# Performance work log

Hardware: AMD Instinct MI355X
Metric: run time of the kernel (lower is better)

The kernel has to match this reference:

```python
import jax, jax.numpy as jnp
import numpy as np

B, C, W, H = 4, 256, 64, 64
DK = C // 8  # query/key channels


def setup_inputs() -> dict:
    key = jax.random.key(0)
    ks = jax.random.split(key, 7)
    x = jax.random.normal(ks[0], (B, C, W, H), dtype=jnp.float32)
    # conv1x1 weights stored as [out_ch, in_ch]
    Wq = jax.random.normal(ks[1], (DK, C), dtype=jnp.float32) / np.sqrt(C)
    bq = jnp.zeros((DK,), dtype=jnp.float32)
    Wk = jax.random.normal(ks[2], (DK, C), dtype=jnp.float32) / np.sqrt(C)
    bk = jnp.zeros((DK,), dtype=jnp.float32)
    Wv = jax.random.normal(ks[3], (C, C), dtype=jnp.float32) / np.sqrt(C)
    bv = jnp.zeros((C,), dtype=jnp.float32)
    gamma = jnp.zeros((1,), dtype=jnp.float32)
    return {"x": x, "Wq": Wq, "bq": bq, "Wk": Wk, "bk": bk,
            "Wv": Wv, "bv": bv, "gamma": gamma}


def reference(x, Wq, bq, Wk, bk, Wv, bv, gamma):
    b, c, w, h = x.shape
    n = w * h
    xf = x.reshape(b, c, n)                     # [B, C, N]
    # conv1x1 == channel matmul
    q = jnp.einsum('dc,bcn->bnd', Wq, xf) + bq  # [B, N, DK]
    k = jnp.einsum('dc,bcn->bdn', Wk, xf) + bk[None, :, None]  # [B, DK, N]
    energy = jnp.einsum('bnd,bdm->bnm', q, k)   # [B, N, N]
    attention = jax.nn.softmax(energy, axis=-1)
    v = jnp.einsum('dc,bcn->bdn', Wv, xf) + bv[None, :, None]  # [B, C, N]
    out = jnp.einsum('bdm,bnm->bdn', v, attention)              # [B, C, N]
    out = out.reshape(b, c, w, h)
    out = gamma * out + x
    return out, attention
```

## Files before the change

kernel.cpp:

```cpp
#include <hip/hip_runtime.h>
#include <hip/hip_bf16.h>

typedef __attribute__((ext_vector_type(8))) short bf16x8;
typedef __attribute__((ext_vector_type(4))) float f32x4;
typedef __attribute__((ext_vector_type(4))) unsigned int u32x4;

#define B_SZ 4
#define C_SZ 256
#define N_SZ 4096
#define DK_SZ 32

#define WQB_OFF 0
#define WKB_OFF 8192
#define WVB_OFF 16384
#define QB_OFF  81920
#define KB_OFF  606208
#define VB_OFF  1130496

__device__ __forceinline__ short f2bf(float f) {
    union { float f; unsigned int u; } v; v.f = f;
    unsigned int r = v.u + 0x7fffu + ((v.u >> 16) & 1u);
    return (short)(r >> 16);
}
__device__ __forceinline__ float bf2f(short s) {
    union { float f; unsigned int u; } v;
    v.u = ((unsigned int)(unsigned short)s) << 16;
    return v.f;
}

__device__ __forceinline__ f32x4 mfma16(bf16x8 a, bf16x8 b, f32x4 c) {
    return __builtin_amdgcn_mfma_f32_16x16x32_bf16(a, b, c, 0, 0, 0);
}

__global__ __launch_bounds__(256) void k_convw(const float* __restrict__ Wq,
                                               const float* __restrict__ Wk,
                                               const float* __restrict__ Wv,
                                               short* __restrict__ ws) {
    int i = blockIdx.x * 256 + threadIdx.x;
    if (i < 8192) {
        ws[WQB_OFF + i] = f2bf(Wq[i]);
        ws[WKB_OFF + i] = f2bf(Wk[i]);
    }
    ws[WVB_OFF + i] = f2bf(Wv[i]);
}

__global__ __launch_bounds__(256) void k_prep(const float* __restrict__ x,
                                              const float* __restrict__ bq,
                                              const float* __restrict__ bk,
                                              const float* __restrict__ bv,
                                              short* __restrict__ ws) {
    __shared__ short xsT[64][264];
    __shared__ short vt_s[64][258];

    const int b = blockIdx.y;
    const int n0 = blockIdx.x * 64;
    const int t = threadIdx.x;
    const float* xb = x + (size_t)b * C_SZ * N_SZ;

    {
        int c0 = t >> 4, n4 = (t & 15) * 4;
#pragma unroll
        for (int i = 0; i < 16; i++) {
            int c = c0 + 16 * i;
            float4 v = *(const float4*)(xb + (size_t)c * N_SZ + n0 + n4);
            xsT[n4 + 0][c] = f2bf(v.x);
            xsT[n4 + 1][c] = f2bf(v.y);
            xsT[n4 + 2][c] = f2bf(v.z);
            xsT[n4 + 3][c] = f2bf(v.w);
        }
    }
    __syncthreads();

    const int w = t >> 6, l = t & 63;
    const int lr = l & 15, lk = l >> 4;

    bf16x8 af[8];
#pragma unroll
    for (int kk = 0; kk < 8; kk++)
        af[kk] = *(const bf16x8*)(&xsT[w * 16 + lr][kk * 32 + lk * 8]);

#pragma unroll
    for (int qk = 0; qk < 2; qk++) {
        const short* wb = ws + (qk ? WKB_OFF : WQB_OFF);
        const float* bias = qk ? bk : bq;
        short* outp = ws + (qk ? KB_OFF : QB_OFF) + (size_t)b * N_SZ * DK_SZ;
#pragma unroll
        for (int cf = 0; cf < 2; cf++) {
            f32x4 acc = {0.f, 0.f, 0.f, 0.f};
#pragma unroll
            for (int kk = 0; kk < 8; kk++) {
                bf16x8 bfr = *(const bf16x8*)(wb + (cf * 16 + lr) * 256 + kk * 32 + lk * 8);
                acc = mfma16(af[kk], bfr, acc);
            }
            float bias_v = bias[cf * 16 + lr];
#pragma unroll
            for (int r = 0; r < 4; r++) {
                int row = w * 16 + lk * 4 + r;
                outp[(size_t)(n0 + row) * DK_SZ + cf * 16 + lr] = f2bf(acc[r] + bias_v);
            }
        }
    }

#pragma unroll
    for (int cf = 0; cf < 16; cf++) {
        f32x4 acc = {0.f, 0.f, 0.f, 0.f};
#pragma unroll
        for (int kk = 0; kk < 8; kk++) {
            bf16x8 bfr = *(const bf16x8*)(ws + WVB_OFF + (cf * 16 + lr) * 256 + kk * 32 + lk * 8);
            acc = mfma16(af[kk], bfr, acc);
        }
        float bias_v = bv[cf * 16 + lr];
#pragma unroll
        for (int r = 0; r < 4; r++) {
            vt_s[w * 16 + lk * 4 + r][cf * 16 + lr] = f2bf(acc[r] + bias_v);
        }
    }
    __syncthreads();
    {
        short* vb = ws + VB_OFF + (size_t)b * C_SZ * N_SZ;
        int nn = t & 63;
#pragma unroll
        for (int i = 0; i < 64; i++) {
            int c = (t >> 6) + 4 * i;
            vb[(size_t)c * N_SZ + n0 + nn] = vt_s[nn][c];
        }
    }
}

__global__ __launch_bounds__(512) void k_attn(const short* __restrict__ ws,
                                              const float* __restrict__ x,
                                              const float* __restrict__ gamma_p,
                                              float* __restrict__ out) {
    __shared__ short v_lds[256][72];
    __shared__ short p_lds[64][72];
    __shared__ float rsum_s[2][64];
    __shared__ float o_s[64][258];

    const int b = blockIdx.y;
    const int n0 = blockIdx.x * 64;
    const int t = threadIdx.x, w = t >> 6, l = t & 63;
    const int rg = w & 3, ch = w >> 2;
    const int lr = l & 15, lk = l >> 4;

    const short* qb = ws + QB_OFF + (size_t)b * N_SZ * DK_SZ;
    const short* kb = ws + KB_OFF + (size_t)b * N_SZ * DK_SZ;
    const short* vb = ws + VB_OFF + (size_t)b * C_SZ * N_SZ;

    bf16x8 qf = *(const bf16x8*)(qb + (size_t)(n0 + rg * 16 + lr) * DK_SZ + lk * 8);

    float rs[4] = {0.f, 0.f, 0.f, 0.f};
    {
        int mb = ch * 32;
        bf16x8 k0 = *(const bf16x8*)(kb + (size_t)(mb + lr) * DK_SZ + lk * 8);
        bf16x8 k1 = *(const bf16x8*)(kb + (size_t)(mb + 16 + lr) * DK_SZ + lk * 8);
        for (int mt = 0; mt < 64; mt++) {
            int mtn = (mt + 1) & 63;
            int mbn = mtn * 64 + ch * 32;
            bf16x8 nk0 = *(const bf16x8*)(kb + (size_t)(mbn + lr) * DK_SZ + lk * 8);
            bf16x8 nk1 = *(const bf16x8*)(kb + (size_t)(mbn + 16 + lr) * DK_SZ + lk * 8);
            f32x4 s0 = {0.f, 0.f, 0.f, 0.f}, s1 = {0.f, 0.f, 0.f, 0.f};
            s0 = mfma16(qf, k0, s0);
            s1 = mfma16(qf, k1, s1);
#pragma unroll
            for (int r = 0; r < 4; r++) rs[r] += __expf(s0[r]) + __expf(s1[r]);
            k0 = nk0; k1 = nk1;
        }
    }
#pragma unroll
    for (int r = 0; r < 4; r++) {
        rs[r] += __shfl_xor(rs[r], 1);
        rs[r] += __shfl_xor(rs[r], 2);
        rs[r] += __shfl_xor(rs[r], 4);
        rs[r] += __shfl_xor(rs[r], 8);
    }
    if (lr == 0) {
#pragma unroll
        for (int r = 0; r < 4; r++) rsum_s[ch][rg * 16 + lk * 4 + r] = rs[r];
    }
    __syncthreads();
    float inv[4];
#pragma unroll
    for (int r = 0; r < 4; r++) {
        int row = rg * 16 + lk * 4 + r;
        inv[r] = 1.f / (rsum_s[0][row] + rsum_s[1][row]);
    }

    float* attn = out + (size_t)B_SZ * C_SZ * N_SZ + (size_t)b * N_SZ * N_SZ;
    f32x4 O[8];
#pragma unroll
    for (int cb = 0; cb < 8; cb++) O[cb] = (f32x4){0.f, 0.f, 0.f, 0.f};

    for (int mt = 0; mt < 64; mt++) {
        int mb = mt * 64;
#pragma unroll
        for (int i = 0; i < 4; i++) {
            int chunk = t + 512 * i;
            int c = chunk >> 3, o8 = chunk & 7;
            u32x4 d = *(const u32x4*)(vb + (size_t)c * N_SZ + mb + o8 * 8);
            *(u32x4*)(&v_lds[c][o8 * 8]) = d;
        }
        {
            int mbh = mb + ch * 32;
            bf16x8 k0 = *(const bf16x8*)(kb + (size_t)(mbh + lr) * DK_SZ + lk * 8);
            bf16x8 k1 = *(const bf16x8*)(kb + (size_t)(mbh + 16 + lr) * DK_SZ + lk * 8);
            f32x4 s0 = {0.f, 0.f, 0.f, 0.f}, s1 = {0.f, 0.f, 0.f, 0.f};
            s0 = mfma16(qf, k0, s0);
            s1 = mfma16(qf, k1, s1);
#pragma unroll
            for (int r = 0; r < 4; r++) {
                int row = rg * 16 + lk * 4 + r;
                p_lds[row][ch * 32 + lr]      = f2bf(__expf(s0[r]) * inv[r]);
                p_lds[row][ch * 32 + 16 + lr] = f2bf(__expf(s1[r]) * inv[r]);
            }
        }
        __syncthreads();
        {
            int n = t >> 3, m8 = (t & 7) * 8;
            bf16x8 pv = *(const bf16x8*)(&p_lds[n][m8]);
            float* dst = attn + (size_t)(n0 + n) * N_SZ + mb + m8;
            float4 f0, f1;
            f0.x = bf2f(pv[0]); f0.y = bf2f(pv[1]); f0.z = bf2f(pv[2]); f0.w = bf2f(pv[3]);
            f1.x = bf2f(pv[4]); f1.y = bf2f(pv[5]); f1.z = bf2f(pv[6]); f1.w = bf2f(pv[7]);
            *(float4*)dst = f0;
            *(float4*)(dst + 4) = f1;
        }
        {
            bf16x8 a0 = *(const bf16x8*)(&p_lds[rg * 16 + lr][lk * 8]);
            bf16x8 a1 = *(const bf16x8*)(&p_lds[rg * 16 + lr][32 + lk * 8]);
#pragma unroll
            for (int cb = 0; cb < 8; cb++) {
                int cc = ch * 128 + cb * 16 + lr;
                bf16x8 b0 = *(const bf16x8*)(&v_lds[cc][lk * 8]);
                bf16x8 b1 = *(const bf16x8*)(&v_lds[cc][32 + lk * 8]);
                O[cb] = mfma16(a0, b0, O[cb]);
                O[cb] = mfma16(a1, b1, O[cb]);
            }
        }
        __syncthreads();
    }

    float g = gamma_p[0];
#pragma unroll
    for (int cb = 0; cb < 8; cb++) {
#pragma unroll
        for (int r = 0; r < 4; r++) {
            o_s[rg * 16 + lk * 4 + r][ch * 128 + cb * 16 + lr] = O[cb][r];
        }
    }
    __syncthreads();
    {
        const float* xb = x + (size_t)b * C_SZ * N_SZ;
        float* ob = out + (size_t)b * C_SZ * N_SZ;
        int nn = t & 63;
#pragma unroll
        for (int i = 0; i < 32; i++) {
            int c = (t >> 6) + 8 * i;
            ob[(size_t)c * N_SZ + n0 + nn] = g * o_s[nn][c] + xb[(size_t)c * N_SZ + n0 + nn];
        }
    }
}

extern "C" void kernel_launch(void* const* d_in, const int* in_sizes, int n_in,
                              void* d_out, int out_size, void* d_ws, size_t ws_size,
                              hipStream_t stream) {
    const float* x     = (const float*)d_in[0];
    const float* Wq    = (const float*)d_in[1];
    const float* bq    = (const float*)d_in[2];
    const float* Wk    = (const float*)d_in[3];
    const float* bk    = (const float*)d_in[4];
    const float* Wv    = (const float*)d_in[5];
    const float* bv    = (const float*)d_in[6];
    const float* gamma = (const float*)d_in[7];
    short* ws = (short*)d_ws;
    float* out = (float*)d_out;

    hipLaunchKernelGGL(k_convw, dim3(256), dim3(256), 0, stream, Wq, Wk, Wv, ws);
    hipLaunchKernelGGL(k_prep, dim3(64, 4), dim3(256), 0, stream, x, bq, bk, bv, ws);
    hipLaunchKernelGGL(k_attn, dim3(64, 4), dim3(512), 0, stream, ws, x, gamma, out);
}
```

Measured before the change: 171.5 us.

## Double-buffer V and P tiles with async global-to-LDS loads in attention kernel

Restructures the attention main loop into a software pipeline. The next V tile is loaded straight into a second LDS buffer with global_load_lds using an XOR-swizzled layout, and the next tile's scores and softmax are computed before the PV MFMAs of the current tile, which removes one barrier per iteration. Attention probabilities are now written to global memory directly from fp32 registers instead of round-tripping through bf16 LDS, and packed bf16 conversion uses v_cvt_pk_bf16_f32. The output staging buffer reuses the V LDS space in two halves to save LDS, and the row-sum pass computes the transposed score tile. The risks are higher register and LDS pressure and the correctness of the swizzle and direct-to-LDS loads.

```diff
diff --git a/kernel.cpp b/kernel.cpp
--- a/kernel.cpp
+++ b/kernel.cpp
@@ -4,6 +4,7 @@
 typedef __attribute__((ext_vector_type(8))) short bf16x8;
 typedef __attribute__((ext_vector_type(4))) float f32x4;
 typedef __attribute__((ext_vector_type(4))) unsigned int u32x4;
+typedef __attribute__((ext_vector_type(2))) unsigned int u32x2;
 
 #define B_SZ 4
 #define C_SZ 256
@@ -22,14 +23,20 @@
     unsigned int r = v.u + 0x7fffu + ((v.u >> 16) & 1u);
     return (short)(r >> 16);
 }
-__device__ __forceinline__ float bf2f(short s) {
-    union { float f; unsigned int u; } v;
-    v.u = ((unsigned int)(unsigned short)s) << 16;
-    return v.f;
+
+__device__ __forceinline__ unsigned int cvt_pk_bf16(float lo, float hi) {
+    unsigned int r;
+    asm volatile("v_cvt_pk_bf16_f32 %0, %1, %2" : "=v"(r) : "v"(lo), "v"(hi));
+    return r;
 }
 
 __device__ __forceinline__ f32x4 mfma16(bf16x8 a, bf16x8 b, f32x4 c) {
     return __builtin_amdgcn_mfma_f32_16x16x32_bf16(a, b, c, 0, 0, 0);
+}
+
+__device__ __forceinline__ void gload_lds16(const void* g, void* l) {
+    __builtin_amdgcn_global_load_lds((const __attribute__((address_space(1))) unsigned int*)g,
+                                     (__attribute__((address_space(3))) unsigned int*)l, 16, 0, 0);
 }
 
 __global__ __launch_bounds__(256) void k_convw(const float* __restrict__ Wq,
@@ -127,14 +134,13 @@
     }
 }
 
-__global__ __launch_bounds__(512) void k_attn(const short* __restrict__ ws,
-                                              const float* __restrict__ x,
-                                              const float* __restrict__ gamma_p,
-                                              float* __restrict__ out) {
-    __shared__ short v_lds[256][72];
-    __shared__ short p_lds[64][72];
+__global__ __launch_bounds__(512, 1) void k_attn(const short* __restrict__ ws,
+                                                 const float* __restrict__ x,
+                                                 const float* __restrict__ gamma_p,
+                                                 float* __restrict__ out) {
+    __shared__ short v_lds[2][256 * 64];
+    __shared__ short p_lds[2][64][72];
     __shared__ float rsum_s[2][64];
-    __shared__ float o_s[64][258];
 
     const int b = blockIdx.y;
     const int n0 = blockIdx.x * 64;
@@ -148,115 +154,115 @@
 
     bf16x8 qf = *(const bf16x8*)(qb + (size_t)(n0 + rg * 16 + lr) * DK_SZ + lk * 8);
 
-    float rs[4] = {0.f, 0.f, 0.f, 0.f};
-    {
-        int mb = ch * 32;
-        bf16x8 k0 = *(const bf16x8*)(kb + (size_t)(mb + lr) * DK_SZ + lk * 8);
-        bf16x8 k1 = *(const bf16x8*)(kb + (size_t)(mb + 16 + lr) * DK_SZ + lk * 8);
-        for (int mt = 0; mt < 64; mt++) {
-            int mtn = (mt + 1) & 63;
-            int mbn = mtn * 64 + ch * 32;
-            bf16x8 nk0 = *(const bf16x8*)(kb + (size_t)(mbn + lr) * DK_SZ + lk * 8);
-            bf16x8 nk1 = *(const bf16x8*)(kb + (size_t)(mbn + 16 + lr) * DK_SZ + lk * 8);
-            f32x4 s0 = {0.f, 0.f, 0.f, 0.f}, s1 = {0.f, 0.f, 0.f, 0.f};
-            s0 = mfma16(qf, k0, s0);
-            s1 = mfma16(qf, k1, s1);
-#pragma unroll
-            for (int r = 0; r < 4; r++) rs[r] += __expf(s0[r]) + __expf(s1[r]);
-            k0 = nk0; k1 = nk1;
-        }
-    }
-#pragma unroll
-    for (int r = 0; r < 4; r++) {
-        rs[r] += __shfl_xor(rs[r], 1);
-        rs[r] += __shfl_xor(rs[r], 2);
-        rs[r] += __shfl_xor(rs[r], 4);
-        rs[r] += __shfl_xor(rs[r], 8);
-    }
-    if (lr == 0) {
-#pragma unroll
-        for (int r = 0; r < 4; r++) rsum_s[ch][rg * 16 + lk * 4 + r] = rs[r];
-    }
-    __syncthreads();
-    float inv[4];
-#pragma unroll
-    for (int r = 0; r < 4; r++) {
-        int row = rg * 16 + lk * 4 + r;
-        inv[r] = 1.f / (rsum_s[0][row] + rsum_s[1][row]);
-    }
+    float rs = 0.f;
+    for (int mt = 0; mt < 32; mt++) {
+        int mb = ch * 2048 + mt * 64;
+        bf16x8 kf0 = *(const bf16x8*)(kb + (size_t)(mb + lr) * DK_SZ + lk * 8);
+        bf16x8 kf1 = *(const bf16x8*)(kb + (size_t)(mb + 16 + lr) * DK_SZ + lk * 8);
+        bf16x8 kf2 = *(const bf16x8*)(kb + (size_t)(mb + 32 + lr) * DK_SZ + lk * 8);
+        bf16x8 kf3 = *(const bf16x8*)(kb + (size_t)(mb + 48 + lr) * DK_SZ + lk * 8);
+        f32x4 s0 = mfma16(kf0, qf, (f32x4){0.f, 0.f, 0.f, 0.f});
+        f32x4 s1 = mfma16(kf1, qf, (f32x4){0.f, 0.f, 0.f, 0.f});
+        f32x4 s2 = mfma16(kf2, qf, (f32x4){0.f, 0.f, 0.f, 0.f});
+        f32x4 s3 = mfma16(kf3, qf, (f32x4){0.f, 0.f, 0.f, 0.f});
+#pragma unroll
+        for (int r = 0; r < 4; r++)
+            rs += __expf(s0[r]) + __expf(s1[r]) + __expf(s2[r]) + __expf(s3[r]);
+    }
+    rs += __shfl_xor(rs, 16);
+    rs += __shfl_xor(rs, 32);
+    if (l < 16) rsum_s[ch][rg * 16 + l] = rs;
+    __syncthreads();
+    const float invp = 1.f / (rsum_s[0][rg * 16 + lr] + rsum_s[1][rg * 16 + lr]);
 
     float* attn = out + (size_t)B_SZ * C_SZ * N_SZ + (size_t)b * N_SZ * N_SZ;
     f32x4 O[8];
 #pragma unroll
     for (int cb = 0; cb < 8; cb++) O[cb] = (f32x4){0.f, 0.f, 0.f, 0.f};
 
+#define SPRIME(tt, pb)                                                                   \
+    {                                                                                    \
+        int mbase = (tt) * 64 + ch * 32;                                                 \
+        _Pragma("unroll")                                                                \
+        for (int t16 = 0; t16 < 2; t16++) {                                              \
+            bf16x8 kf = *(const bf16x8*)(kb + (size_t)(mbase + t16 * 16 + lr) * DK_SZ + lk * 8); \
+            f32x4 s = mfma16(kf, qf, (f32x4){0.f, 0.f, 0.f, 0.f});                       \
+            float4 e;                                                                    \
+            e.x = __expf(s[0]) * invp; e.y = __expf(s[1]) * invp;                        \
+            e.z = __expf(s[2]) * invp; e.w = __expf(s[3]) * invp;                        \
+            *(float4*)(attn + (size_t)(n0 + rg * 16 + lr) * N_SZ + mbase + t16 * 16 + lk * 4) = e; \
+            u32x2 pk;                                                                    \
+            pk[0] = cvt_pk_bf16(e.x, e.y);                                               \
+            pk[1] = cvt_pk_bf16(e.z, e.w);                                               \
+            *(u32x2*)(&p_lds[pb][rg * 16 + lr][ch * 32 + t16 * 16 + lk * 4]) = pk;       \
+        }                                                                                \
+    }
+
+#define STAGE(tt, vbuf)                                                                  \
+    {                                                                                    \
+        int mb = (tt) * 64;                                                              \
+        _Pragma("unroll")                                                                \
+        for (int i = 0; i < 4; i++) {                                                    \
+            int c = w * 32 + i * 8 + (l >> 3);                                           \
+            int j = l & 7;                                                               \
+            const short* g = vb + (size_t)c * N_SZ + mb + ((j ^ (c & 7)) << 3);          \
+            gload_lds16(g, (void*)&v_lds[vbuf][(w * 32 + i * 8) * 64]);                  \
+        }                                                                                \
+    }
+
+    STAGE(0, 0);
+    SPRIME(0, 0);
+
     for (int mt = 0; mt < 64; mt++) {
-        int mb = mt * 64;
-#pragma unroll
-        for (int i = 0; i < 4; i++) {
-            int chunk = t + 512 * i;
-            int c = chunk >> 3, o8 = chunk & 7;
-            u32x4 d = *(const u32x4*)(vb + (size_t)c * N_SZ + mb + o8 * 8);
-            *(u32x4*)(&v_lds[c][o8 * 8]) = d;
-        }
-        {
-            int mbh = mb + ch * 32;
-            bf16x8 k0 = *(const bf16x8*)(kb + (size_t)(mbh + lr) * DK_SZ + lk * 8);
-            bf16x8 k1 = *(const bf16x8*)(kb + (size_t)(mbh + 16 + lr) * DK_SZ + lk * 8);
-            f32x4 s0 = {0.f, 0.f, 0.f, 0.f}, s1 = {0.f, 0.f, 0.f, 0.f};
-            s0 = mfma16(qf, k0, s0);
-            s1 = mfma16(qf, k1, s1);
-#pragma unroll
-            for (int r = 0; r < 4; r++) {
-                int row = rg * 16 + lk * 4 + r;
-                p_lds[row][ch * 32 + lr]      = f2bf(__expf(s0[r]) * inv[r]);
-                p_lds[row][ch * 32 + 16 + lr] = f2bf(__expf(s1[r]) * inv[r]);
+        __syncthreads();
+        int cur = mt & 1;
+        if (mt < 63) {
+            STAGE(mt + 1, cur ^ 1);
+            SPRIME(mt + 1, cur ^ 1);
+        }
+        const char* pbase = (const char*)&p_lds[cur][rg * 16 + lr][0];
+        bf16x8 pa0 = *(const bf16x8*)(pbase + lk * 16);
+        bf16x8 pa1 = *(const bf16x8*)(pbase + 64 + lk * 16);
+        const char* vbase = (const char*)&v_lds[cur][0];
+#pragma unroll
+        for (int cb = 0; cb < 8; cb++) {
+            int c = ch * 128 + cb * 16 + lr;
+            int sw = (c & 7) << 4;
+            bf16x8 b0 = *(const bf16x8*)(vbase + c * 128 + ((lk << 4) ^ sw));
+            bf16x8 b1 = *(const bf16x8*)(vbase + c * 128 + (((4 + lk) << 4) ^ sw));
+            O[cb] = mfma16(pa0, b0, O[cb]);
+            O[cb] = mfma16(pa1, b1, O[cb]);
+        }
+    }
+
+    __syncthreads();
+    const float g = gamma_p[0];
+    float* o_s = (float*)&v_lds[0][0];
+    const float* xb = x + (size_t)b * C_SZ * N_SZ;
+    float* ob = out + (size_t)b * C_SZ * N_SZ;
+#pragma unroll
+    for (int half = 0; half < 2; half++) {
+        if ((rg >> 1) == half) {
+#pragma unroll
+            for (int cb = 0; cb < 8; cb++) {
+#pragma unroll
+                for (int r = 0; r < 4; r++) {
+                    o_s[((rg & 1) * 16 + lk * 4 + r) * 258 + ch * 128 + cb * 16 + lr] = O[cb][r];
+                }
             }
         }
         __syncthreads();
         {
-            int n = t >> 3, m8 = (t & 7) * 8;
-            bf16x8 pv = *(const bf16x8*)(&p_lds[n][m8]);
-            float* dst = attn + (size_t)(n0 + n) * N_SZ + mb + m8;
-            float4 f0, f1;
-            f0.x = bf2f(pv[0]); f0.y = bf2f(pv[1]); f0.z = bf2f(pv[2]); f0.w = bf2f(pv[3]);
-            f1.x = bf2f(pv[4]); f1.y = bf2f(pv[5]); f1.z = bf2f(pv[6]); f1.w = bf2f(pv[7]);
-            *(float4*)dst = f0;
-            *(float4*)(dst + 4) = f1;
-        }
-        {
-            bf16x8 a0 = *(const bf16x8*)(&p_lds[rg * 16 + lr][lk * 8]);
-            bf16x8 a1 = *(const bf16x8*)(&p_lds[rg * 16 + lr][32 + lk * 8]);
-#pragma unroll
-            for (int cb = 0; cb < 8; cb++) {
-                int cc = ch * 128 + cb * 16 + lr;
-                bf16x8 b0 = *(const bf16x8*)(&v_lds[cc][lk * 8]);
-                bf16x8 b1 = *(const bf16x8*)(&v_lds[cc][32 + lk * 8]);
-                O[cb] = mfma16(a0, b0, O[cb]);
-                O[cb] = mfma16(a1, b1, O[cb]);
+            int nn = t & 31;
+            int c0 = t >> 5;
+#pragma unroll
+            for (int i = 0; i < 16; i++) {
+                int c = c0 + 16 * i;
+                size_t idx = (size_t)c * N_SZ + n0 + half * 32 + nn;
+                ob[idx] = g * o_s[nn * 258 + c] + xb[idx];
             }
         }
         __syncthreads();
-    }
-
-    float g = gamma_p[0];
-#pragma unroll
-    for (int cb = 0; cb < 8; cb++) {
-#pragma unroll
-        for (int r = 0; r < 4; r++) {
-            o_s[rg * 16 + lk * 4 + r][ch * 128 + cb * 16 + lr] = O[cb][r];
-        }
-    }
-    __syncthreads();
-    {
-        const float* xb = x + (size_t)b * C_SZ * N_SZ;
-        float* ob = out + (size_t)b * C_SZ * N_SZ;
-        int nn = t & 63;
-#pragma unroll
-        for (int i = 0; i < 32; i++) {
-            int c = (t >> 6) + 8 * i;
-            ob[(size_t)c * N_SZ + n0 + nn] = g * o_s[nn][c] + xb[(size_t)c * N_SZ + n0 + nn];
-        }
     }
 }
 
```

New measurement: 166.0 us. -3.2%, faster.
